# Kernel optimization log

Hardware: AMD Instinct MI355X
Metric: run time of the kernel (lower is better)

Reference implementation:

```python
import jax, jax.numpy as jnp
import numpy as np

N, IN_C, HID, E = 100000, 1024, 128, 1600000


def setup_inputs() -> dict:
    key = jax.random.key(0)
    k1, k2, k3 = jax.random.split(key, 3)
    x = jax.random.normal(k1, (N, IN_C), dtype=jnp.float32)
    # GCNConv weight (bias=False), applied as x @ W : [in, hidden]
    W = jax.random.normal(k2, (IN_C, HID), dtype=jnp.float32) * (1.0 / np.sqrt(IN_C))
    edge_index = jax.random.randint(k3, (2, E), 0, N, dtype=jnp.int64)
    return {"x": x, "W": W, "edge_index": edge_index}


def reference(x, W, edge_index):
    n = x.shape[0]
    row, col = edge_index[0], edge_index[1]  # src -> dst
    # add self-loops (PyG GCNConv default)
    loop = jnp.arange(n, dtype=edge_index.dtype)
    row = jnp.concatenate([row, loop])
    col = jnp.concatenate([col, loop])
    # symmetric normalization: deg on destination, includes self-loops (deg >= 1)
    deg = jax.ops.segment_sum(jnp.ones(col.shape, jnp.float32), col, num_segments=n)
    dinv = jax.lax.rsqrt(deg)
    norm = dinv[row] * dinv[col]  # [E+N]
    # linear transform first (in -> hidden), then gather/scale/scatter-add
    h = x @ W                      # [N, HID]
    msg = h[row] * norm[:, None]   # [E+N, HID]
    out = jax.ops.segment_sum(msg, col, num_segments=n)  # [N, HID]
    return out
```

## Files before the change

kernel.cpp:

```cpp
#include <hip/hip_runtime.h>
#include <hip/hip_bf16.h>

#define NN 100000
#define INC 1024
#define HID 128
#define NE 1600000
#define NB ((NN + 255) / 256)

typedef float floatx4 __attribute__((ext_vector_type(4)));
typedef __bf16 bf16x8 __attribute__((ext_vector_type(8)));
typedef unsigned short ushort8v __attribute__((ext_vector_type(8)));
typedef unsigned short ushort4v __attribute__((ext_vector_type(4)));

__device__ __forceinline__ unsigned short f2bf(float f) {
    union { float f; unsigned u; } v; v.f = f;
    unsigned r = v.u + 0x7fffu + ((v.u >> 16) & 1u);
    return (unsigned short)(r >> 16);
}

__global__ __launch_bounds__(256) void init_cnt_k(int* cnt) {
    int i = blockIdx.x * 256 + threadIdx.x;
    if (i < NN) cnt[i] = 0;
}

__global__ __launch_bounds__(256) void deg_edges_k(const int* __restrict__ col, int* cnt) {
    int e = blockIdx.x * 256 + threadIdx.x;
    if (e < NE) atomicAdd(&cnt[col[e]], 1);
}

__global__ __launch_bounds__(256) void dinv_k(const int* __restrict__ cnt, float* __restrict__ dinv) {
    int i = blockIdx.x * 256 + threadIdx.x;
    if (i < NN) dinv[i] = rsqrtf((float)(cnt[i] + 1));
}

__global__ __launch_bounds__(256) void scan1_k(const int* __restrict__ cnt,
                                               int* __restrict__ excl, int* __restrict__ bsum) {
    __shared__ int sh[256];
    const int t = threadIdx.x, b = blockIdx.x;
    const int idx = b * 256 + t;
    const int v = (idx < NN) ? cnt[idx] : 0;
    sh[t] = v;
    __syncthreads();
#pragma unroll
    for (int off = 1; off < 256; off <<= 1) {
        const int x = sh[t];
        const int y = (t >= off) ? sh[t - off] : 0;
        __syncthreads();
        sh[t] = x + y;
        __syncthreads();
    }
    if (idx < NN) excl[idx] = sh[t] - v;
    if (t == 255) bsum[b] = sh[255];
}

__global__ __launch_bounds__(512) void scan2_k(const int* __restrict__ bsum, int* __restrict__ boff) {
    __shared__ int sh[512];
    const int t = threadIdx.x;
    const int v = (t < NB) ? bsum[t] : 0;
    sh[t] = v;
    __syncthreads();
#pragma unroll
    for (int off = 1; off < 512; off <<= 1) {
        const int x = sh[t];
        const int y = (t >= off) ? sh[t - off] : 0;
        __syncthreads();
        sh[t] = x + y;
        __syncthreads();
    }
    if (t < NB) boff[t] = sh[t] - v;
}

__global__ __launch_bounds__(256) void scan3_k(const int* __restrict__ excl, const int* __restrict__ boff,
                                               int* __restrict__ rowptr, int* __restrict__ cursor) {
    const int idx = blockIdx.x * 256 + threadIdx.x;
    if (idx < NN) {
        const int v = excl[idx] + boff[blockIdx.x];
        rowptr[idx] = v;
        cursor[idx] = v;
    }
    if (idx == 0) rowptr[NN] = NE;
}

__global__ __launch_bounds__(256) void fill_k(const int* __restrict__ ei,
                                              int* cursor, int* __restrict__ ssrc) {
    const int e = blockIdx.x * 256 + threadIdx.x;
    if (e < NE) {
        const int r = ei[e];
        const int c = ei[NE + e];
        const int pos = atomicAdd(&cursor[c], 1);
        ssrc[pos] = r;
    }
}

__global__ __launch_bounds__(256) void wt_k(const float* __restrict__ W, unsigned short* __restrict__ Wt) {
    int idx = blockIdx.x * 256 + threadIdx.x;
    int n = idx >> 10, k = idx & 1023;
    Wt[idx] = f2bf(W[k * HID + n]);
}

__global__ __launch_bounds__(256) void gemm_hp_k(
    const float* __restrict__ x, const unsigned short* __restrict__ Wt,
    const float* __restrict__ dinv, float* __restrict__ hp)
{
    __shared__ unsigned short As[64 * 40];
    __shared__ unsigned short Bs[128 * 40];
    const int tid  = threadIdx.x;
    const int lane = tid & 63;
    const int wave = tid >> 6;
    const int q    = lane >> 4;
    const int l16  = lane & 15;
    const int brow = blockIdx.x * 64;

    floatx4 acc[8];
#pragma unroll
    for (int t = 0; t < 8; ++t) acc[t] = (floatx4){0.f, 0.f, 0.f, 0.f};

    for (int k0 = 0; k0 < INC; k0 += 32) {
        {
            const int m  = tid >> 3;
            const int kk = (tid & 7) * 4;
#pragma unroll
            for (int h = 0; h < 2; ++h) {
                const int mm = m + h * 32;
                const int g  = brow + mm;
                float4 v = make_float4(0.f, 0.f, 0.f, 0.f);
                if (g < NN) v = *(const float4*)&x[(size_t)g * INC + k0 + kk];
                ushort4v w;
                w.x = f2bf(v.x); w.y = f2bf(v.y); w.z = f2bf(v.z); w.w = f2bf(v.w);
                *(ushort4v*)&As[mm * 40 + kk] = w;
            }
        }
        {
            const int n  = tid >> 1;
            const int kk = (tid & 1) * 16;
            ushort8v a = *(const ushort8v*)&Wt[(size_t)n * INC + k0 + kk];
            ushort8v b = *(const ushort8v*)&Wt[(size_t)n * INC + k0 + kk + 8];
            *(ushort8v*)&Bs[n * 40 + kk]     = a;
            *(ushort8v*)&Bs[n * 40 + kk + 8] = b;
        }
        __syncthreads();

        const bf16x8 af = *(const bf16x8*)&As[(wave * 16 + l16) * 40 + q * 8];
#pragma unroll
        for (int t = 0; t < 8; ++t) {
            const bf16x8 bf = *(const bf16x8*)&Bs[(t * 16 + l16) * 40 + q * 8];
            acc[t] = __builtin_amdgcn_mfma_f32_16x16x32_bf16(af, bf, acc[t], 0, 0, 0);
        }
        __syncthreads();
    }

#pragma unroll
    for (int r = 0; r < 4; ++r) {
        const int row = brow + wave * 16 + q * 4 + r;
        if (row < NN) {
            const float d = dinv[row];
#pragma unroll
            for (int t = 0; t < 8; ++t) {
                const int col = t * 16 + l16;
                hp[(size_t)row * HID + col] = acc[t][r] * d;
            }
        }
    }
}

__global__ __launch_bounds__(256) void agg_k(const int* __restrict__ rowptr,
                                             const int* __restrict__ ssrc,
                                             const float* __restrict__ hp,
                                             const float* __restrict__ dinv,
                                             float* __restrict__ out)
{
    const int w = (blockIdx.x * 256 + threadIdx.x) >> 6;
    const int lane = threadIdx.x & 63;
    if (w >= NN) return;
    const int s = rowptr[w];
    const int e = rowptr[w + 1];
    const size_t loff = (size_t)lane * 2;

    const float2 self = *(const float2*)&hp[(size_t)w * HID + loff];
    float ax = self.x, ay = self.y;

    for (int i = s; i < e; i += 64) {
        const int rem = e - i;
        const int cnt = rem < 64 ? rem : 64;
        int srcv = 0;
        if (lane < rem) srcv = ssrc[i + lane];
        int j = 0;
        for (; j + 4 <= cnt; j += 4) {
            const int s0 = __shfl(srcv, j + 0);
            const int s1 = __shfl(srcv, j + 1);
            const int s2 = __shfl(srcv, j + 2);
            const int s3 = __shfl(srcv, j + 3);
            const float2 v0 = *(const float2*)&hp[(size_t)s0 * HID + loff];
            const float2 v1 = *(const float2*)&hp[(size_t)s1 * HID + loff];
            const float2 v2 = *(const float2*)&hp[(size_t)s2 * HID + loff];
            const float2 v3 = *(const float2*)&hp[(size_t)s3 * HID + loff];
            ax += v0.x + v1.x + v2.x + v3.x;
            ay += v0.y + v1.y + v2.y + v3.y;
        }
        for (; j < cnt; ++j) {
            const int sj = __shfl(srcv, j);
            const float2 v = *(const float2*)&hp[(size_t)sj * HID + loff];
            ax += v.x;
            ay += v.y;
        }
    }

    const float d = dinv[w];
    float2 r;
    r.x = ax * d;
    r.y = ay * d;
    *(float2*)&out[(size_t)w * HID + loff] = r;
}

extern "C" void kernel_launch(void* const* d_in, const int* in_sizes, int n_in,
                              void* d_out, int out_size, void* d_ws, size_t ws_size,
                              hipStream_t stream) {
    const float* x  = (const float*)d_in[0];
    const float* W  = (const float*)d_in[1];
    const int*   ei = (const int*)d_in[2];
    float* out = (float*)d_out;

    char* p = (char*)d_ws;
    float* hp      = (float*)p;            p += (size_t)NN * HID * 4;
    int*   cnt     = (int*)p;              p += (size_t)NN * 4;
    int*   rowptr  = (int*)p;              p += (size_t)(NN + 4) * 4;
    int*   cursor  = (int*)p;              p += (size_t)NN * 4;
    int*   excl    = (int*)p;              p += (size_t)NN * 4;
    float* dinv    = (float*)p;            p += (size_t)NN * 4;
    unsigned short* Wt = (unsigned short*)p; p += (size_t)INC * HID * 2;
    int*   bsum    = (int*)p;              p += 512 * 4;
    int*   boff    = (int*)p;              p += 512 * 4;
    int*   ssrc    = (int*)p;              p += (size_t)NE * 4;

    init_cnt_k <<<NB, 256, 0, stream>>>(cnt);
    deg_edges_k<<<(NE + 255) / 256, 256, 0, stream>>>(ei + NE, cnt);
    dinv_k     <<<NB, 256, 0, stream>>>(cnt, dinv);
    scan1_k    <<<NB, 256, 0, stream>>>(cnt, excl, bsum);
    scan2_k    <<<1, 512, 0, stream>>>(bsum, boff);
    scan3_k    <<<NB, 256, 0, stream>>>(excl, boff, rowptr, cursor);
    fill_k     <<<(NE + 255) / 256, 256, 0, stream>>>(ei, cursor, ssrc);
    wt_k       <<<(INC * HID) / 256, 256, 0, stream>>>(W, Wt);
    gemm_hp_k  <<<(NN + 63) / 64, 256, 0, stream>>>(x, Wt, dinv, hp);
    agg_k      <<<(NN * 64 + 255) / 256, 256, 0, stream>>>(rowptr, ssrc, hp, dinv, out);
}
```

Baseline: 908.3 us.

## Load GEMM operands directly into MFMA registers, drop LDS staging; unroll gather by 8

The GEMM no longer stages x and W tiles through shared memory with two barriers per k-step. Each lane loads its bf16 fragments straight from global memory, and each wave computes two 16-row tiles, so a block covers 128 rows. This removes LDS traffic and synchronisation and reuses each B fragment across two row tiles. The cost is uncoalesced 32-byte strided global loads of x, with W fragments re-read from L2 by every wave. The aggregation loop is also unrolled to 8 neighbours per iteration, giving more gathers in flight.

```diff
diff --git a/kernel.cpp b/kernel.cpp
--- a/kernel.cpp
+++ b/kernel.cpp
@@ -10,7 +10,6 @@
 typedef float floatx4 __attribute__((ext_vector_type(4)));
 typedef __bf16 bf16x8 __attribute__((ext_vector_type(8)));
 typedef unsigned short ushort8v __attribute__((ext_vector_type(8)));
-typedef unsigned short ushort4v __attribute__((ext_vector_type(4)));
 
 __device__ __forceinline__ unsigned short f2bf(float f) {
     union { float f; unsigned u; } v; v.f = f;
@@ -102,62 +101,64 @@
     const float* __restrict__ x, const unsigned short* __restrict__ Wt,
     const float* __restrict__ dinv, float* __restrict__ hp)
 {
-    __shared__ unsigned short As[64 * 40];
-    __shared__ unsigned short Bs[128 * 40];
     const int tid  = threadIdx.x;
     const int lane = tid & 63;
     const int wave = tid >> 6;
     const int q    = lane >> 4;
     const int l16  = lane & 15;
-    const int brow = blockIdx.x * 64;
-
-    floatx4 acc[8];
-#pragma unroll
-    for (int t = 0; t < 8; ++t) acc[t] = (floatx4){0.f, 0.f, 0.f, 0.f};
+    const int brow = blockIdx.x * 128;
+
+    floatx4 acc[2][8];
+#pragma unroll
+    for (int rt = 0; rt < 2; ++rt)
+#pragma unroll
+        for (int t = 0; t < 8; ++t) acc[rt][t] = (floatx4){0.f, 0.f, 0.f, 0.f};
+
+    const int r0 = brow + wave * 32 + l16;
+    const int r1 = r0 + 16;
+    const int c0 = (r0 < NN) ? r0 : (NN - 1);
+    const int c1 = (r1 < NN) ? r1 : (NN - 1);
+    const float* xp0 = x + (size_t)c0 * INC;
+    const float* xp1 = x + (size_t)c1 * INC;
+    const unsigned short* wp = Wt + (size_t)l16 * INC;
 
     for (int k0 = 0; k0 < INC; k0 += 32) {
-        {
-            const int m  = tid >> 3;
-            const int kk = (tid & 7) * 4;
-#pragma unroll
-            for (int h = 0; h < 2; ++h) {
-                const int mm = m + h * 32;
-                const int g  = brow + mm;
-                float4 v = make_float4(0.f, 0.f, 0.f, 0.f);
-                if (g < NN) v = *(const float4*)&x[(size_t)g * INC + k0 + kk];
-                ushort4v w;
-                w.x = f2bf(v.x); w.y = f2bf(v.y); w.z = f2bf(v.z); w.w = f2bf(v.w);
-                *(ushort4v*)&As[mm * 40 + kk] = w;
-            }
-        }
-        {
-            const int n  = tid >> 1;
-            const int kk = (tid & 1) * 16;
-            ushort8v a = *(const ushort8v*)&Wt[(size_t)n * INC + k0 + kk];
-            ushort8v b = *(const ushort8v*)&Wt[(size_t)n * INC + k0 + kk + 8];
-            *(ushort8v*)&Bs[n * 40 + kk]     = a;
-            *(ushort8v*)&Bs[n * 40 + kk + 8] = b;
-        }
-        __syncthreads();
-
-        const bf16x8 af = *(const bf16x8*)&As[(wave * 16 + l16) * 40 + q * 8];
+        const int ko = k0 + q * 8;
+        const float4 a0l = *(const float4*)(xp0 + ko);
+        const float4 a0h = *(const float4*)(xp0 + ko + 4);
+        const float4 a1l = *(const float4*)(xp1 + ko);
+        const float4 a1h = *(const float4*)(xp1 + ko + 4);
+
+        union { ushort8v u; bf16x8 b; } af0, af1;
+        af0.u[0] = f2bf(a0l.x); af0.u[1] = f2bf(a0l.y); af0.u[2] = f2bf(a0l.z); af0.u[3] = f2bf(a0l.w);
+        af0.u[4] = f2bf(a0h.x); af0.u[5] = f2bf(a0h.y); af0.u[6] = f2bf(a0h.z); af0.u[7] = f2bf(a0h.w);
+        af1.u[0] = f2bf(a1l.x); af1.u[1] = f2bf(a1l.y); af1.u[2] = f2bf(a1l.z); af1.u[3] = f2bf(a1l.w);
+        af1.u[4] = f2bf(a1h.x); af1.u[5] = f2bf(a1h.y); af1.u[6] = f2bf(a1h.z); af1.u[7] = f2bf(a1h.w);
+
+        bf16x8 bf[8];
+#pragma unroll
+        for (int t = 0; t < 8; ++t)
+            bf[t] = *(const bf16x8*)(wp + (size_t)t * 16 * INC + ko);
+
 #pragma unroll
         for (int t = 0; t < 8; ++t) {
-            const bf16x8 bf = *(const bf16x8*)&Bs[(t * 16 + l16) * 40 + q * 8];
-            acc[t] = __builtin_amdgcn_mfma_f32_16x16x32_bf16(af, bf, acc[t], 0, 0, 0);
-        }
-        __syncthreads();
-    }
-
-#pragma unroll
-    for (int r = 0; r < 4; ++r) {
-        const int row = brow + wave * 16 + q * 4 + r;
-        if (row < NN) {
-            const float d = dinv[row];
-#pragma unroll
-            for (int t = 0; t < 8; ++t) {
-                const int col = t * 16 + l16;
-                hp[(size_t)row * HID + col] = acc[t][r] * d;
+            acc[0][t] = __builtin_amdgcn_mfma_f32_16x16x32_bf16(af0.b, bf[t], acc[0][t], 0, 0, 0);
+            acc[1][t] = __builtin_amdgcn_mfma_f32_16x16x32_bf16(af1.b, bf[t], acc[1][t], 0, 0, 0);
+        }
+    }
+
+#pragma unroll
+    for (int rt = 0; rt < 2; ++rt) {
+#pragma unroll
+        for (int r = 0; r < 4; ++r) {
+            const int row = brow + wave * 32 + rt * 16 + q * 4 + r;
+            if (row < NN) {
+                const float d = dinv[row];
+#pragma unroll
+                for (int t = 0; t < 8; ++t) {
+                    const int col = t * 16 + l16;
+                    hp[(size_t)row * HID + col] = acc[rt][t][r] * d;
+                }
             }
         }
     }
@@ -185,17 +186,25 @@
         int srcv = 0;
         if (lane < rem) srcv = ssrc[i + lane];
         int j = 0;
-        for (; j + 4 <= cnt; j += 4) {
+        for (; j + 8 <= cnt; j += 8) {
             const int s0 = __shfl(srcv, j + 0);
             const int s1 = __shfl(srcv, j + 1);
             const int s2 = __shfl(srcv, j + 2);
             const int s3 = __shfl(srcv, j + 3);
+            const int s4 = __shfl(srcv, j + 4);
+            const int s5 = __shfl(srcv, j + 5);
+            const int s6 = __shfl(srcv, j + 6);
+            const int s7 = __shfl(srcv, j + 7);
             const float2 v0 = *(const float2*)&hp[(size_t)s0 * HID + loff];
             const float2 v1 = *(const float2*)&hp[(size_t)s1 * HID + loff];
             const float2 v2 = *(const float2*)&hp[(size_t)s2 * HID + loff];
             const float2 v3 = *(const float2*)&hp[(size_t)s3 * HID + loff];
-            ax += v0.x + v1.x + v2.x + v3.x;
-            ay += v0.y + v1.y + v2.y + v3.y;
+            const float2 v4 = *(const float2*)&hp[(size_t)s4 * HID + loff];
+            const float2 v5 = *(const float2*)&hp[(size_t)s5 * HID + loff];
+            const float2 v6 = *(const float2*)&hp[(size_t)s6 * HID + loff];
+            const float2 v7 = *(const float2*)&hp[(size_t)s7 * HID + loff];
+            ax += v0.x + v1.x + v2.x + v3.x + v4.x + v5.x + v6.x + v7.x;
+            ay += v0.y + v1.y + v2.y + v3.y + v4.y + v5.y + v6.y + v7.y;
         }
         for (; j < cnt; ++j) {
             const int sj = __shfl(srcv, j);
@@ -240,6 +249,6 @@
     scan3_k    <<<NB, 256, 0, stream>>>(excl, boff, rowptr, cursor);
     fill_k     <<<(NE + 255) / 256, 256, 0, stream>>>(ei, cursor, ssrc);
     wt_k       <<<(INC * HID) / 256, 256, 0, stream>>>(W, Wt);
-    gemm_hp_k  <<<(NN + 63) / 64, 256, 0, stream>>>(x, Wt, dinv, hp);
+    gemm_hp_k  <<<(NN + 127) / 128, 256, 0, stream>>>(x, Wt, dinv, hp);
     agg_k      <<<(NN * 64 + 255) / 256, 256, 0, stream>>>(rowptr, ssrc, hp, dinv, out);
 }
```

Result: slower. 982.7 us (+8.2%).
